# Kernel optimization log

Measured on AMD Instinct MI355X. Metric: run time of the kernel, lower is better.

Reference implementation:

```python
import jax, jax.numpy as jnp
import numpy as np
import math

B, N, D = 8, 2048, 1024
DK = D // 4
TOP_K = 32
SCALE = math.sqrt(DK)
NEG = -1000000000.0


def setup_inputs() -> dict:
    key = jax.random.key(0)
    k1, k2, k3, k4, k5 = jax.random.split(key, 5)
    lim = 1.0 / math.sqrt(D)
    return {
        "action_states": jax.random.normal(k1, (B, N, D), dtype=jnp.float32),
        "Wq": jax.random.uniform(k2, (D, DK), minval=-lim, maxval=lim, dtype=jnp.float32),
        "bq": jax.random.uniform(k3, (DK,), minval=-lim, maxval=lim, dtype=jnp.float32),
        "Wk": jax.random.uniform(k4, (D, DK), minval=-lim, maxval=lim, dtype=jnp.float32),
        "bk": jax.random.uniform(k5, (DK,), minval=-lim, maxval=lim, dtype=jnp.float32),
    }


def reference(action_states, Wq, bq, Wk, bk):
    # Q, K projections: (B, N, DK)
    Q = jnp.einsum("bnd,dk->bnk", action_states, Wq) + bq
    K = jnp.einsum("bnd,dk->bnk", action_states, Wk) + bk
    # scaled dot-product scores: (B, N, N)
    scores = jnp.einsum("bqk,bmk->bqm", Q, K) / SCALE
    # top-k sparsify per row + scatter mask
    topk_vals, topk_idx = jax.lax.top_k(scores, TOP_K)  # (B, N, K)
    bi = jnp.arange(B)[:, None, None]
    ni = jnp.arange(N)[None, :, None]
    mask = jnp.zeros_like(scores).at[bi, ni, topk_idx].set(1.0)
    scores = scores * mask + (1.0 - mask) * NEG
    return jax.nn.softmax(scores, axis=-1)
```

## Files before the change

kernel.cpp:

```cpp
#include <hip/hip_runtime.h>
#include <cstdint>
#include <cstddef>

#define B_   8
#define N_   2048
#define D_   1024
#define DK_  256
#define M_   (B_ * N_)
#define TOPK 32
#define NDIG 5

typedef unsigned short ushort_t;
typedef float  fvec4 __attribute__((ext_vector_type(4)));
typedef short  bvec8 __attribute__((ext_vector_type(8)));
typedef float  avec4 __attribute__((ext_vector_type(4)));
typedef int    ivec4 __attribute__((ext_vector_type(4)));

__device__ inline ushort_t f32_to_bf16_rn(float f) {
  unsigned u = __float_as_uint(f);
  u += 0x7fffu + ((u >> 16) & 1u);
  return (ushort_t)(u >> 16);
}
__device__ inline float bf16_to_f32(ushort_t u) {
  return __uint_as_float(((unsigned)u) << 16);
}
__device__ inline unsigned bf16_key(ushort_t h) {
  return (h & 0x8000u) ? (unsigned)((~h) & 0xFFFFu) : (unsigned)(h | 0x8000u);
}
__device__ inline float key_to_f32(unsigned k) {
  const ushort_t h = (k & 0x8000u) ? (ushort_t)(k ^ 0x8000u)
                                   : (ushort_t)((~k) & 0xFFFFu);
  return bf16_to_f32(h);
}

__global__ __launch_bounds__(256) void split_x_kernel(
    const float* __restrict__ X, signed char* __restrict__ Xdig)
{
  const size_t MK = (size_t)M_ * D_;
  const int total = (int)(MK / 4);
  for (int idx = blockIdx.x * 256 + threadIdx.x; idx < total;
       idx += gridDim.x * 256) {
    const fvec4 x = ((const fvec4*)X)[idx];
    unsigned pack[NDIG] = {0u, 0u, 0u, 0u, 0u};
#pragma unroll
    for (int e = 0; e < 4; e++) {
      float s = x[e] * 0.0625f * 128.f;
#pragma unroll
      for (int d = 0; d < NDIG; d++) {
        const float a = rintf(s);
        s = (s - a) * 128.f;
        pack[d] |= ((unsigned)((int)a & 0xff)) << (e * 8);
      }
    }
#pragma unroll
    for (int d = 0; d < NDIG; d++)
      ((unsigned*)(Xdig + (size_t)d * MK))[idx] = pack[d];
  }
}

__global__ __launch_bounds__(256) void split_w_kernel(
    const float* __restrict__ Wq, const float* __restrict__ Wk,
    signed char* __restrict__ Wdig)
{
  const size_t WK = (size_t)512 * 1024;
  const int cc = blockIdx.x;
  const float* Wp = (cc < 256) ? Wq : Wk;
  const int c = cc & 255;
  const int k0 = threadIdx.x * 4;
  unsigned pack[NDIG] = {0u, 0u, 0u, 0u, 0u};
#pragma unroll
  for (int e = 0; e < 4; e++) {
    float s = Wp[(size_t)(k0 + e) * DK_ + c] * 16.f * 128.f;
#pragma unroll
    for (int d = 0; d < NDIG; d++) {
      const float a = rintf(s);
      s = (s - a) * 128.f;
      pack[d] |= ((unsigned)((int)a & 0xff)) << (e * 8);
    }
  }
#pragma unroll
  for (int d = 0; d < NDIG; d++)
    ((unsigned*)(Wdig + (size_t)d * WK + (size_t)cc * 1024))[threadIdx.x] = pack[d];
}

__global__ __launch_bounds__(512) void ozaki_gemm_kernel(
    const signed char* __restrict__ Xdig, const signed char* __restrict__ Wdig,
    const float* __restrict__ bq, const float* __restrict__ bk,
    double* __restrict__ Qd, double* __restrict__ Kd,
    ushort_t* __restrict__ Qbf, ushort_t* __restrict__ Kbf)
{
  __shared__ __align__(16) char L[61440];
  const int tid  = threadIdx.x;
  const int lane = tid & 63;
  const int w    = tid >> 6;
  const int wm   = (w >> 2) * 32;
  const int wc   = (w & 3) * 32;
  const int m0   = blockIdx.y * 64;
  const int c0   = blockIdx.x * 128;
  const size_t MK = (size_t)M_ * D_;
  const size_t WK = (size_t)512 * 1024;

  ivec4 acc[NDIG][2][2];
#pragma unroll
  for (int s = 0; s < NDIG; s++)
#pragma unroll
    for (int mi = 0; mi < 2; mi++)
#pragma unroll
      for (int nj = 0; nj < 2; nj++) acc[s][mi][nj] = (ivec4)(0);

  for (int k0 = 0; k0 < D_; k0 += 64) {
    for (int c = tid; c < 1280; c += 512) {
      const int d = c >> 8, rem = c & 255, r = rem >> 2, kp = rem & 3;
      const ivec4 raw = *(const ivec4*)(Xdig + (size_t)d * MK +
                         (size_t)(m0 + r) * D_ + k0 + kp * 16);
      *(ivec4*)&L[d * 4096 + r * 64 + ((kp ^ (r & 3)) << 4)] = raw;
    }
    for (int c = tid; c < 2560; c += 512) {
      const int d = c >> 9, rem = c & 511, r = rem >> 2, kp = rem & 3;
      const ivec4 raw = *(const ivec4*)(Wdig + (size_t)d * WK +
                         (size_t)(c0 + r) * 1024 + k0 + kp * 16);
      *(ivec4*)&L[20480 + d * 8192 + r * 64 + ((kp ^ (r & 3)) << 4)] = raw;
    }
    __syncthreads();

    ivec4 afr[2][NDIG];
#pragma unroll
    for (int mi = 0; mi < 2; mi++) {
      const int r = wm + mi * 16 + (lane & 15);
      const int sl = (((lane >> 4) ^ (r & 3)) << 4);
#pragma unroll
      for (int d = 0; d < NDIG; d++)
        afr[mi][d] = *(const ivec4*)&L[d * 4096 + r * 64 + sl];
    }
#pragma unroll
    for (int nj = 0; nj < 2; nj++) {
      const int rc = wc + nj * 16 + (lane & 15);
      const int sl = (((lane >> 4) ^ (rc & 3)) << 4);
#pragma unroll
      for (int jd = 0; jd < NDIG; jd++) {
        const ivec4 bfr = *(const ivec4*)&L[20480 + jd * 8192 + rc * 64 + sl];
#pragma unroll
        for (int id = 0; id + jd < NDIG; id++)
#pragma unroll
          for (int mi = 0; mi < 2; mi++)
            acc[id + jd][mi][nj] = __builtin_amdgcn_mfma_i32_16x16x64_i8(
                afr[mi][id], bfr, acc[id + jd][mi][nj], 0, 0, 0);
      }
    }
    __syncthreads();
  }

  const double SCL[NDIG] = {0x1p-14, 0x1p-21, 0x1p-28, 0x1p-35, 0x1p-42};
#pragma unroll
  for (int nj = 0; nj < 2; nj++) {
    const int c = c0 + wc + nj * 16 + (lane & 15);
    const bool isQ = (c < 256);
    const int cw = isQ ? c : (c - 256);
    const double bias = (double)(isQ ? bq[cw] : bk[cw]);
#pragma unroll
    for (int mi = 0; mi < 2; mi++) {
#pragma unroll
      for (int ri = 0; ri < 4; ri++) {
        const int m = m0 + wm + mi * 16 + (lane >> 4) * 4 + ri;
        double val = bias;
#pragma unroll
        for (int s = 0; s < NDIG; s++)
          val += (double)acc[s][mi][nj][ri] * SCL[s];
        const size_t off = (size_t)m * DK_ + cw;
        if (isQ) { Qd[off] = val; Qbf[off] = f32_to_bf16_rn((float)val); }
        else     { Kd[off] = val; Kbf[off] = f32_to_bf16_rn((float)val); }
      }
    }
  }
}

__global__ __launch_bounds__(256) void proj_kernel(
    const float* __restrict__ X, const float* __restrict__ Wq,
    const float* __restrict__ bq, const float* __restrict__ Wk,
    const float* __restrict__ bk, double* __restrict__ Qd,
    double* __restrict__ Kd, ushort_t* __restrict__ Qbf,
    ushort_t* __restrict__ Kbf)
{
  __shared__ float As[16][132];
  __shared__ float Bs[16][132];
  const int tid = threadIdx.x;
  const int tx = tid & 15;
  const int ty = tid >> 4;
  const int m0 = blockIdx.y * 128;
  const int j0 = blockIdx.x * 128;
  const bool isQ = (j0 < 256);
  const float* Wp = isQ ? Wq : Wk;
  const float* bp = isQ ? bq : bk;
  const int jw = isQ ? j0 : (j0 - 256);

  double acc[8][8];
#pragma unroll
  for (int i = 0; i < 8; i++)
#pragma unroll
    for (int j = 0; j < 8; j++) acc[i][j] = 0.0;

  for (int k0 = 0; k0 < D_; k0 += 16) {
    {
      const int r = tid >> 2, k4 = (tid & 3) * 4;
#pragma unroll
      for (int p = 0; p < 2; p++) {
        const int m = r + 64 * p;
        const fvec4 v = *(const fvec4*)&X[(size_t)(m0 + m) * D_ + k0 + k4];
#pragma unroll
        for (int c = 0; c < 4; c++) As[k4 + c][m] = v[c];
      }
    }
    {
      const int k = tid >> 4, j8 = (tid & 15) * 8;
      const fvec4 v0 = *(const fvec4*)&Wp[(size_t)(k0 + k) * DK_ + jw + j8];
      const fvec4 v1 = *(const fvec4*)&Wp[(size_t)(k0 + k) * DK_ + jw + j8 + 4];
      *(fvec4*)&Bs[k][j8]     = v0;
      *(fvec4*)&Bs[k][j8 + 4] = v1;
    }
    __syncthreads();
#pragma unroll
    for (int kk = 0; kk < 16; kk++) {
      const fvec4 a0 = *(const fvec4*)&As[kk][ty * 8];
      const fvec4 a1 = *(const fvec4*)&As[kk][ty * 8 + 4];
      const fvec4 b0 = *(const fvec4*)&Bs[kk][tx * 8];
      const fvec4 b1 = *(const fvec4*)&Bs[kk][tx * 8 + 4];
      double a[8], b[8];
#pragma unroll
      for (int i = 0; i < 4; i++) {
        a[i] = (double)a0[i]; a[i + 4] = (double)a1[i];
        b[i] = (double)b0[i]; b[i + 4] = (double)b1[i];
      }
#pragma unroll
      for (int i = 0; i < 8; i++)
#pragma unroll
        for (int j = 0; j < 8; j++)
          acc[i][j] = fma(a[i], b[j], acc[i][j]);
    }
    __syncthreads();
  }

#pragma unroll
  for (int i = 0; i < 8; i++) {
    const int m = m0 + ty * 8 + i;
#pragma unroll
    for (int j = 0; j < 8; j++) {
      const int c = jw + tx * 8 + j;
      const double v = acc[i][j] + (double)bp[c];
      const size_t off = (size_t)m * DK_ + c;
      if (isQ) { Qd[off] = v; if (Qbf) Qbf[off] = f32_to_bf16_rn((float)v); }
      else     { Kd[off] = v; if (Kbf) Kbf[off] = f32_to_bf16_rn((float)v); }
    }
  }
}

__global__ __launch_bounds__(256) void score_bf16_kernel(
    const ushort_t* __restrict__ Qb, const ushort_t* __restrict__ Kb,
    float* __restrict__ outf, ushort_t* __restrict__ outbf)
{
  __shared__ ushort_t Asl[128 * 40];
  __shared__ ushort_t Bsl[128 * 40];
  const int tid = threadIdx.x;
  const int b  = blockIdx.z;
  const int q0 = blockIdx.y * 128;
  const int m0 = blockIdx.x * 128;
  const int w = tid >> 6, lane = tid & 63;
  const int wq = (w >> 1) * 64, wm = (w & 1) * 64;
  const int rsel = lane & 15, ksel = (lane >> 4) * 8;

  avec4 acc[4][4];
#pragma unroll
  for (int i = 0; i < 4; i++)
#pragma unroll
    for (int j = 0; j < 4; j++) acc[i][j] = (avec4)(0.f);

  for (int k0 = 0; k0 < DK_; k0 += 32) {
#pragma unroll
    for (int cc = 0; cc < 2; cc++) {
      const int c = tid + cc * 256;
      const int r = c >> 2, part = c & 3;
      const ivec4 va = *(const ivec4*)&Qb[((size_t)b * N_ + q0 + r) * DK_ + k0 + part * 8];
      const ivec4 vb = *(const ivec4*)&Kb[((size_t)b * N_ + m0 + r) * DK_ + k0 + part * 8];
      *(ivec4*)&Asl[r * 40 + part * 8] = va;
      *(ivec4*)&Bsl[r * 40 + part * 8] = vb;
    }
    __syncthreads();
    bvec8 aF[4], bF[4];
#pragma unroll
    for (int mi = 0; mi < 4; mi++)
      aF[mi] = *(const bvec8*)&Asl[(wq + mi * 16 + rsel) * 40 + ksel];
#pragma unroll
    for (int nj = 0; nj < 4; nj++)
      bF[nj] = *(const bvec8*)&Bsl[(wm + nj * 16 + rsel) * 40 + ksel];
#pragma unroll
    for (int mi = 0; mi < 4; mi++)
#pragma unroll
      for (int nj = 0; nj < 4; nj++)
        acc[mi][nj] = __builtin_amdgcn_mfma_f32_16x16x32_bf16(
            aF[mi], bF[nj], acc[mi][nj], 0, 0, 0);
    __syncthreads();
  }

#pragma unroll
  for (int mi = 0; mi < 4; mi++)
#pragma unroll
    for (int nj = 0; nj < 4; nj++)
#pragma unroll
      for (int r = 0; r < 4; r++) {
        const int row = q0 + wq + mi * 16 + (lane >> 4) * 4 + r;
        const int col = m0 + wm + nj * 16 + (lane & 15);
        const size_t off = ((size_t)b * N_ + row) * N_ + col;
        const float v = acc[mi][nj][r] * 0.0625f;
        if (outbf) outbf[off] = f32_to_bf16_rn(v);
        else       outf[off] = v;
      }
}

__global__ __launch_bounds__(256) void score_f64_kernel(
    const double* __restrict__ Qd, const double* __restrict__ Kd,
    float* __restrict__ out)
{
  __shared__ float As[16][68];
  __shared__ float Bs[16][68];
  const int tid = threadIdx.x;
  const int tx = tid & 15, ty = tid >> 4;
  const int b  = blockIdx.z;
  const int q0 = blockIdx.y * 64;
  const int m0 = blockIdx.x * 64;
  const size_t rowbase = (size_t)b * N_;

  float acc[4][4];
#pragma unroll
  for (int i = 0; i < 4; i++)
#pragma unroll
    for (int j = 0; j < 4; j++) acc[i][j] = 0.f;

  for (int k0 = 0; k0 < DK_; k0 += 16) {
    const int mt = tid >> 4, kt = tid & 15;
#pragma unroll
    for (int p = 0; p < 4; p++) {
      const int m = mt + 16 * p;
      As[kt][m] = (float)Qd[(rowbase + q0 + m) * DK_ + k0 + kt];
      Bs[kt][m] = (float)Kd[(rowbase + m0 + m) * DK_ + k0 + kt];
    }
    __syncthreads();
#pragma unroll
    for (int kk = 0; kk < 16; kk++) {
      float a[4], bb[4];
#pragma unroll
      for (int i = 0; i < 4; i++) a[i] = As[kk][ty * 4 + i];
#pragma unroll
      for (int j = 0; j < 4; j++) bb[j] = Bs[kk][tx * 4 + j];
#pragma unroll
      for (int i = 0; i < 4; i++)
#pragma unroll
        for (int j = 0; j < 4; j++)
          acc[i][j] = fmaf(a[i], bb[j], acc[i][j]);
    }
    __syncthreads();
  }

#pragma unroll
  for (int i = 0; i < 4; i++) {
    const size_t r = (size_t)b * N_ + q0 + ty * 4 + i;
#pragma unroll
    for (int j = 0; j < 4; j++)
      out[r * N_ + m0 + tx * 4 + j] = acc[i][j] * 0.0625f;
  }
}

__global__ __launch_bounds__(256) void topk_scatter_kernel(
    float* __restrict__ out, const ushort_t* __restrict__ sbf,
    const double* __restrict__ Qd, const double* __restrict__ Kd,
    float margin)
{
  const int bid = blockIdx.x;
  const int row = (bid & 7) * 2048 + (bid >> 3);
  const int b   = row >> 11;
  const int tid = threadIdx.x;
  const int lane = tid & 63, wid = tid >> 6;

  __shared__ double   qrow[DK_];
  __shared__ int      cidx[128];
  __shared__ double   cval[128];
  __shared__ int      cnt_ws[4];
  __shared__ int      ncand_s;
  __shared__ double   wmax[4];
  __shared__ float    wsum[4];

  const ivec4 v = *(const ivec4*)&sbf[(size_t)row * N_ + tid * 8];
  const ushort_t* u = (const ushort_t*)&v;
  unsigned kk[8];
  float    fv[8];
#pragma unroll
  for (int e = 0; e < 8; e++) {
    kk[e] = bf16_key(u[e]);
    fv[e] = bf16_to_f32(u[e]);
  }
  qrow[tid] = Qd[(size_t)row * DK_ + tid];
  if (tid == 0) ncand_s = 0;

  unsigned lo = 0, hi = 65535;
#pragma unroll 1
  for (int it = 0; it < 16; it++) {
    const unsigned mid = (lo + hi + 1) >> 1;
    int c = 0;
#pragma unroll
    for (int e = 0; e < 8; e++) c += (kk[e] >= mid);
#pragma unroll
    for (int off = 32; off > 0; off >>= 1) c += __shfl_xor(c, off);
    if (lane == 0) cnt_ws[wid] = c;
    __syncthreads();
    const int tot = cnt_ws[0] + cnt_ws[1] + cnt_ws[2] + cnt_ws[3];
    if (tot >= TOPK) lo = mid; else hi = mid - 1;
    __syncthreads();
  }
  const float cthr = key_to_f32(lo) - margin;

#pragma unroll
  for (int e = 0; e < 8; e++) {
    if (fv[e] >= cthr) {
      const int p = atomicAdd(&ncand_s, 1);
      if (p < 128) cidx[p] = tid * 8 + e;
    }
  }
  __syncthreads();
  int nc = ncand_s;
  if (nc > 128) nc = 128;

  for (int base = 0; base < nc; base += 4) {
    const int c = base + wid;
    if (c < nc) {
      const double* kp = Kd + ((size_t)b * N_ + cidx[c]) * DK_;
      double a = 0.0;
#pragma unroll
      for (int q = 0; q < 4; q++)
        a = fma(qrow[lane * 4 + q], kp[lane * 4 + q], a);
#pragma unroll
      for (int off = 32; off > 0; off >>= 1) a += __shfl_xor(a, off);
      if (lane == 0) cval[c] = a * 0.0625;
    }
  }
  __syncthreads();

  bool sel = false;
  double vv = 0.0;
  int myidx = 0;
  if (tid < nc) {
    vv = cval[tid];
    myidx = cidx[tid];
    int rank = 0;
    for (int j = 0; j < nc; j++) {
      const double vj = cval[j];
      rank += (vj > vv) || (vj == vv && cidx[j] < myidx);
    }
    sel = (rank < TOPK);
  }
  double mv = (tid < nc) ? vv : -1.0e300;
#pragma unroll
  for (int off = 32; off > 0; off >>= 1) {
    const double o = __shfl_xor(mv, off);
    mv = o > mv ? o : mv;
  }
  if (lane == 0) wmax[wid] = mv;
  __syncthreads();
  const double vmax = max(max(wmax[0], wmax[1]), max(wmax[2], wmax[3]));
  const float ev = sel ? expf((float)(vv - vmax)) : 0.f;
  float es = ev;
#pragma unroll
  for (int off = 32; off > 0; off >>= 1) es += __shfl_xor(es, off);
  if (lane == 0) wsum[wid] = es;
  __syncthreads();
  const float esum = wsum[0] + wsum[1] + wsum[2] + wsum[3];

  if (sel) out[(size_t)row * N_ + myidx] = ev / esum;
}

__global__ __launch_bounds__(256) void topk_softmax_kernel(
    float* __restrict__ out, const ushort_t* __restrict__ sbf,
    const float* __restrict__ sf, const double* __restrict__ Qd,
    const double* __restrict__ Kd, float margin)
{
  const int row = blockIdx.x;
  const int b   = row >> 11;
  const int tid = threadIdx.x;
  float* rowp = out + (size_t)row * N_;

  __shared__ float    s[N_];
  __shared__ double   qrow[DK_];
  __shared__ unsigned hist[256];
  __shared__ unsigned sfx[256];
  __shared__ int      cidx[128];
  __shared__ double   cval[128];
  __shared__ int      ncand_s;
  __shared__ unsigned prefix_s;
  __shared__ int      want_s;
  __shared__ double   wmax[4];
  __shared__ float    wsum[4];

  if (sbf) {
    const ivec4 v = *(const ivec4*)&sbf[(size_t)row * N_ + tid * 8];
    const ushort_t* u = (const ushort_t*)&v;
#pragma unroll
    for (int c = 0; c < 8; c++) s[tid * 8 + c] = bf16_to_f32(u[c]);
  } else {
#pragma unroll
    for (int p = 0; p < 2; p++) {
      const fvec4 v = *(const fvec4*)&sf[(size_t)row * N_ + tid * 8 + p * 4];
#pragma unroll
      for (int c = 0; c < 4; c++) s[tid * 8 + p * 4 + c] = v[c];
    }
  }
  qrow[tid] = Qd[(size_t)row * DK_ + tid];
  __syncthreads();

  unsigned prefix = 0;
  int want = TOPK;
  for (int pass = 0; pass < 2; pass++) {
    hist[tid] = 0;
    __syncthreads();
    const int shift_b = 8 - 8 * pass;
    for (int i = tid; i < N_; i += 256) {
      unsigned uu = __float_as_uint(s[i]);
      uu = (uu & 0x80000000u) ? ~uu : (uu | 0x80000000u);
      const unsigned key = uu >> 16;
      const bool ok = (pass == 0) || ((key >> 8) == prefix);
      if (ok) atomicAdd(&hist[(key >> shift_b) & 255u], 1u);
    }
    __syncthreads();
    sfx[tid] = hist[tid];
    __syncthreads();
    for (int st = 1; st < 256; st <<= 1) {
      const unsigned add = (tid + st < 256) ? sfx[tid + st] : 0u;
      __syncthreads();
      sfx[tid] += add;
      __syncthreads();
    }
    const int gt = (int)(sfx[tid] - hist[tid]);
    if (gt < want && (int)sfx[tid] >= want) {
      prefix_s = (prefix << 8) | (unsigned)tid;
      want_s = want - gt;
    }
    __syncthreads();
    prefix = prefix_s;
    want = want_s;
    __syncthreads();
  }
  const unsigned k16 = prefix;
  unsigned ulo;
  if (k16 & 0x8000u) ulo = (k16 << 16) ^ 0x80000000u;
  else               ulo = ~(k16 << 16);
  const float cthr = __uint_as_float(ulo) - margin;

  if (tid == 0) ncand_s = 0;
  __syncthreads();
  for (int i = tid; i < N_; i += 256) {
    if (s[i] >= cthr) {
      const int p = atomicAdd(&ncand_s, 1);
      if (p < 128) cidx[p] = i;
    }
  }
  __syncthreads();
  int nc = ncand_s;
  if (nc > 128) nc = 128;

  const int wid = tid >> 6, lane = tid & 63;
  for (int base = 0; base < nc; base += 4) {
    const int c = base + wid;
    if (c < nc) {
      const double* kp = Kd + ((size_t)b * N_ + cidx[c]) * DK_;
      double a = 0.0;
#pragma unroll
      for (int q = 0; q < 4; q++)
        a = fma(qrow[lane * 4 + q], kp[lane * 4 + q], a);
#pragma unroll
      for (int off = 32; off > 0; off >>= 1) a += __shfl_xor(a, off);
      if (lane == 0) cval[c] = a * 0.0625;
    }
  }
  __syncthreads();

  bool sel = false;
  double v = 0.0;
  int myidx = 0;
  if (tid < nc) {
    v = cval[tid];
    myidx = cidx[tid];
    int rank = 0;
    for (int j = 0; j < nc; j++) {
      const double vj = cval[j];
      rank += (vj > v) || (vj == v && cidx[j] < myidx);
    }
    sel = (rank < TOPK);
  }
  double mv = (tid < nc) ? v : -1.0e300;
#pragma unroll
  for (int off = 32; off > 0; off >>= 1) {
    const double o = __shfl_xor(mv, off);
    mv = o > mv ? o : mv;
  }
  if (lane == 0) wmax[wid] = mv;
  __syncthreads();
  const double vmax = max(max(wmax[0], wmax[1]), max(wmax[2], wmax[3]));
  const float ev = sel ? expf((float)(v - vmax)) : 0.f;
  float es = ev;
#pragma unroll
  for (int off = 32; off > 0; off >>= 1) es += __shfl_xor(es, off);
  if (lane == 0) wsum[wid] = es;
  __syncthreads();
  const float esum = wsum[0] + wsum[1] + wsum[2] + wsum[3];

  for (int i = tid; i < N_; i += 256) s[i] = 0.f;
  __syncthreads();
  if (sel) s[myidx] = ev / esum;
  __syncthreads();
  for (int i = tid; i < N_; i += 256) rowp[i] = s[i];
}

extern "C" void kernel_launch(void* const* d_in, const int* in_sizes, int n_in,
                              void* d_out, int out_size, void* d_ws,
                              size_t ws_size, hipStream_t stream)
{
  const float* X  = (const float*)d_in[0];
  const float* Wq = (const float*)d_in[1];
  const float* bq = (const float*)d_in[2];
  const float* Wk = (const float*)d_in[3];
  const float* bk = (const float*)d_in[4];
  float* out = (float*)d_out;

  const size_t qk = (size_t)M_ * DK_;
  const size_t f64_bytes  = qk * 8 * 2;
  const size_t bf_bytes   = qk * 2 * 2;
  const size_t base       = f64_bytes + bf_bytes;
  const size_t xdig_bytes = (size_t)M_ * D_ * NDIG;
  const size_t wdig_bytes = (size_t)512 * 1024 * NDIG;
  const size_t sbf_bytes  = (size_t)M_ * N_ * 2;
  const size_t oz_total = base + xdig_bytes + wdig_bytes;
  const size_t sc_total = base + sbf_bytes;
  if (ws_size < f64_bytes) return;

  double* Qd = (double*)d_ws;
  double* Kd = Qd + qk;
  ushort_t* Qbf = (ushort_t*)(Kd + qk);
  ushort_t* Kbf = Qbf + qk;
  char* region = (char*)d_ws + base;

  dim3 blk(256);
  if (ws_size >= oz_total) {
    signed char* Xdig = (signed char*)region;
    signed char* Wdig = Xdig + xdig_bytes;
    hipMemsetAsync(out, 0, (size_t)M_ * N_ * sizeof(float), stream);
    split_x_kernel<<<2048, blk, 0, stream>>>(X, Xdig);
    split_w_kernel<<<512, blk, 0, stream>>>(Wq, Wk, Wdig);
    ozaki_gemm_kernel<<<dim3(4, 256), dim3(512), 0, stream>>>(
        Xdig, Wdig, bq, bk, Qd, Kd, Qbf, Kbf);
    score_bf16_kernel<<<dim3(N_ / 128, N_ / 128, B_), blk, 0, stream>>>(
        Qbf, Kbf, out, (ushort_t*)region);
    topk_scatter_kernel<<<dim3(M_), blk, 0, stream>>>(
        out, (ushort_t*)region, Qd, Kd, 2.5e-2f);
    return;
  }

  const bool bfpath = (ws_size >= base);
  const bool scpath = (ws_size >= sc_total);
  proj_kernel<<<dim3(4, 128), blk, 0, stream>>>(
      X, Wq, bq, Wk, bk, Qd, Kd, bfpath ? Qbf : (ushort_t*)nullptr,
      bfpath ? Kbf : (ushort_t*)nullptr);
  if (bfpath) {
    score_bf16_kernel<<<dim3(N_ / 128, N_ / 128, B_), blk, 0, stream>>>(
        Qbf, Kbf, out, scpath ? (ushort_t*)region : (ushort_t*)nullptr);
    if (scpath)
      topk_softmax_kernel<<<dim3(M_), blk, 0, stream>>>(
          out, (ushort_t*)region, (const float*)nullptr, Qd, Kd, 1.6e-2f);
    else
      topk_softmax_kernel<<<dim3(M_), blk, 0, stream>>>(
          out, (const ushort_t*)nullptr, out, Qd, Kd, 8e-3f);
  } else {
    score_f64_kernel<<<dim3(N_ / 64, N_ / 64, B_), blk, 0, stream>>>(Qd, Kd, out);
    topk_softmax_kernel<<<dim3(M_), blk, 0, stream>>>(
        out, (const ushort_t*)nullptr, out, Qd, Kd, 2.5e-4f);
  }
}
```

Before: 512.3 us.

## Fuse output zeroing into score kernel and retile candidate rescoring in top-k

```diff
diff --git a/kernel.cpp b/kernel.cpp
--- a/kernel.cpp
+++ b/kernel.cpp
@@ -267,6 +267,14 @@
   const int wq = (w >> 1) * 64, wm = (w & 1) * 64;
   const int rsel = lane & 15, ksel = (lane >> 4) * 8;
 
+  if (outf && outbf) {
+    const fvec4 z = (fvec4)(0.f);
+    for (int i = tid; i < 4096; i += 256) {
+      const int r = i >> 5, c4 = i & 31;
+      *(fvec4*)&outf[((size_t)b * N_ + q0 + r) * N_ + m0 + c4 * 4] = z;
+    }
+  }
+
   avec4 acc[4][4];
 #pragma unroll
   for (int i = 0; i < 4; i++)
@@ -378,11 +386,11 @@
   const int b   = row >> 11;
   const int tid = threadIdx.x;
   const int lane = tid & 63, wid = tid >> 6;
-
-  __shared__ double   qrow[DK_];
+  const int grp = tid >> 4, l4 = tid & 15;
+
   __shared__ int      cidx[128];
   __shared__ double   cval[128];
-  __shared__ int      cnt_ws[4];
+  __shared__ int      cnt_ws[2][4];
   __shared__ int      ncand_s;
   __shared__ double   wmax[4];
   __shared__ float    wsum[4];
@@ -396,7 +404,10 @@
     kk[e] = bf16_key(u[e]);
     fv[e] = bf16_to_f32(u[e]);
   }
-  qrow[tid] = Qd[(size_t)row * DK_ + tid];
+  double qreg[16];
+#pragma unroll
+  for (int q = 0; q < 16; q++)
+    qreg[q] = Qd[(size_t)row * DK_ + q * 16 + l4];
   if (tid == 0) ncand_s = 0;
 
   unsigned lo = 0, hi = 65535;
@@ -408,11 +419,11 @@
     for (int e = 0; e < 8; e++) c += (kk[e] >= mid);
 #pragma unroll
     for (int off = 32; off > 0; off >>= 1) c += __shfl_xor(c, off);
-    if (lane == 0) cnt_ws[wid] = c;
-    __syncthreads();
-    const int tot = cnt_ws[0] + cnt_ws[1] + cnt_ws[2] + cnt_ws[3];
+    if (lane == 0) cnt_ws[it & 1][wid] = c;
+    __syncthreads();
+    const int tot = cnt_ws[it & 1][0] + cnt_ws[it & 1][1] +
+                    cnt_ws[it & 1][2] + cnt_ws[it & 1][3];
     if (tot >= TOPK) lo = mid; else hi = mid - 1;
-    __syncthreads();
   }
   const float cthr = key_to_f32(lo) - margin;
 
@@ -427,17 +438,17 @@
   int nc = ncand_s;
   if (nc > 128) nc = 128;
 
-  for (int base = 0; base < nc; base += 4) {
-    const int c = base + wid;
+  for (int base = 0; base < nc; base += 16) {
+    const int c = base + grp;
     if (c < nc) {
       const double* kp = Kd + ((size_t)b * N_ + cidx[c]) * DK_;
       double a = 0.0;
 #pragma unroll
-      for (int q = 0; q < 4; q++)
-        a = fma(qrow[lane * 4 + q], kp[lane * 4 + q], a);
-#pragma unroll
-      for (int off = 32; off > 0; off >>= 1) a += __shfl_xor(a, off);
-      if (lane == 0) cval[c] = a * 0.0625;
+      for (int q = 0; q < 16; q++)
+        a = fma(qreg[q], kp[q * 16 + l4], a);
+#pragma unroll
+      for (int off = 1; off < 16; off <<= 1) a += __shfl_xor(a, off);
+      if (l4 == 0) cval[c] = a * 0.0625;
     }
   }
   __syncthreads();
@@ -648,7 +659,6 @@
   if (ws_size >= oz_total) {
     signed char* Xdig = (signed char*)region;
     signed char* Wdig = Xdig + xdig_bytes;
-    hipMemsetAsync(out, 0, (size_t)M_ * N_ * sizeof(float), stream);
     split_x_kernel<<<2048, blk, 0, stream>>>(X, Xdig);
     split_w_kernel<<<512, blk, 0, stream>>>(Wq, Wk, Wdig);
     ozaki_gemm_kernel<<<dim3(4, 256), dim3(512), 0, stream>>>(
@@ -656,7 +666,7 @@
     score_bf16_kernel<<<dim3(N_ / 128, N_ / 128, B_), blk, 0, stream>>>(
         Qbf, Kbf, out, (ushort_t*)region);
     topk_scatter_kernel<<<dim3(M_), blk, 0, stream>>>(
-        out, (ushort_t*)region, Qd, Kd, 2.5e-2f);
+        out, (ushort_t*)region, Qd, Kd, 1.6e-2f);
     return;
   }
 
@@ -667,7 +677,8 @@
       bfpath ? Kbf : (ushort_t*)nullptr);
   if (bfpath) {
     score_bf16_kernel<<<dim3(N_ / 128, N_ / 128, B_), blk, 0, stream>>>(
-        Qbf, Kbf, out, scpath ? (ushort_t*)region : (ushort_t*)nullptr);
+        Qbf, Kbf, scpath ? (float*)nullptr : out,
+        scpath ? (ushort_t*)region : (ushort_t*)nullptr);
     if (scpath)
       topk_softmax_kernel<<<dim3(M_), blk, 0, stream>>>(
           out, (ushort_t*)region, (const float*)nullptr, Qd, Kd, 1.6e-2f);
```

New measurement: 481.9 us. 1.06x faster.
